# Optimization experiments

Measured on AMD Instinct MI355X. Metric: run time of the kernel, lower is better.

The kernel has to match this reference:

```python
import jax, jax.numpy as jnp
import numpy as np

EMA_W = 0.99


def setup_inputs() -> dict:
    key = jax.random.key(0)
    k1, k2 = jax.random.split(key)
    B, C, H, W = 16, 8, 512, 512
    generated_masks = jax.random.normal(k1, (B, C, H, W), dtype=jnp.float32)
    prev_dist = jax.random.uniform(k2, (C,), dtype=jnp.float32)
    prev_dist = prev_dist / jnp.sum(prev_dist)  # a valid running distribution
    return {"generated_masks": generated_masks, "prev_dist": prev_dist}


def reference(generated_masks, prev_dist):
    # generated_masks: [B, C, H, W]; prev_dist: [C]
    B, C, H, W = generated_masks.shape
    num_classes = C
    norm_factor = 1.0 / num_classes

    # per-pixel argmax over channels -> [B, H, W]
    mask_classes = jnp.argmax(generated_masks, axis=1)

    # histogram over classes (fused equivalent of torch.unique + scatter)
    hist = jnp.zeros((num_classes,), dtype=jnp.float32).at[
        mask_classes.reshape(-1)
    ].add(1.0)

    total = B * H * W
    class_distribution = prev_dist * EMA_W + (1.0 - EMA_W) * hist / total

    balance = jnp.linalg.norm(
        (class_distribution - norm_factor) / (1.0 - norm_factor)
    )
    return balance, class_distribution
```

## Files before the change

kernel.cpp:

```cpp
#include <hip/hip_runtime.h>
#include <math.h>

#define HW      262144
#define HWQ     65536
#define CHW     2097152
#define NGROUPS 1048576
#define NBLOCKS 1024
#define NTHREADS 256
#define TOTAL_PX 4194304.0f

__global__ __launch_bounds__(NTHREADS)
void argmax_hist_kernel(const float* __restrict__ masks,
                        unsigned int* __restrict__ partial) {
    const int tid = threadIdx.x;
    int cnt[8] = {0, 0, 0, 0, 0, 0, 0, 0};

    for (int g = blockIdx.x * NTHREADS + tid; g < NGROUPS; g += NBLOCKS * NTHREADS) {
        const int b   = g >> 16;
        const int hw4 = (g & 65535) << 2;
        const float4* p = (const float4*)(masks + (size_t)b * CHW + hw4);

        float4 v = p[0];
        float bv0 = v.x, bv1 = v.y, bv2 = v.z, bv3 = v.w;
        int   bi0 = 0,   bi1 = 0,   bi2 = 0,   bi3 = 0;
        #pragma unroll
        for (int c = 1; c < 8; ++c) {
            float4 u = p[(size_t)c * HWQ];
            bi0 = (u.x > bv0) ? c : bi0;  bv0 = (u.x > bv0) ? u.x : bv0;
            bi1 = (u.y > bv1) ? c : bi1;  bv1 = (u.y > bv1) ? u.y : bv1;
            bi2 = (u.z > bv2) ? c : bi2;  bv2 = (u.z > bv2) ? u.z : bv2;
            bi3 = (u.w > bv3) ? c : bi3;  bv3 = (u.w > bv3) ? u.w : bv3;
        }
        #pragma unroll
        for (int k = 0; k < 8; ++k) {
            cnt[k] += (bi0 == k) + (bi1 == k) + (bi2 == k) + (bi3 == k);
        }
    }

    #pragma unroll
    for (int k = 0; k < 8; ++k) {
        #pragma unroll
        for (int off = 32; off >= 1; off >>= 1) {
            cnt[k] += __shfl_down(cnt[k], off, 64);
        }
    }

    __shared__ int lds[32];
    const int lane = tid & 63;
    const int wid  = tid >> 6;
    if (lane == 0) {
        #pragma unroll
        for (int k = 0; k < 8; ++k) lds[wid * 8 + k] = cnt[k];
    }
    __syncthreads();
    if (tid < 8) {
        unsigned int s = (unsigned int)(lds[tid] + lds[8 + tid] + lds[16 + tid] + lds[24 + tid]);
        partial[blockIdx.x * 8 + tid] = s;
    }
}

__global__ __launch_bounds__(64)
void finalize_kernel(const unsigned int* __restrict__ partial,
                     const float* __restrict__ prev,
                     float* __restrict__ out) {
    __shared__ float s[64];
    const int t = threadIdx.x;
    const int c = t & 7;
    const int r = t >> 3;

    unsigned int sum = 0;
    for (int row = r; row < NBLOCKS; row += 8) {
        sum += partial[row * 8 + c];
    }
    s[t] = (float)sum;
    __syncthreads();

    if (t < 8) {
        float h = 0.0f;
        #pragma unroll
        for (int k = 0; k < 8; ++k) h += s[t + 8 * k];
        float dist = prev[t] * 0.99f + 0.01f * h / TOTAL_PX;
        out[1 + t] = dist;
        float d = (dist - 0.125f) / 0.875f;
        s[t] = d * d;
    }
    __syncthreads();
    if (t == 0) {
        float acc = 0.0f;
        #pragma unroll
        for (int k = 0; k < 8; ++k) acc += s[k];
        out[0] = sqrtf(acc);
    }
}

extern "C" void kernel_launch(void* const* d_in, const int* in_sizes, int n_in,
                              void* d_out, int out_size, void* d_ws, size_t ws_size,
                              hipStream_t stream) {
    const float* masks = (const float*)d_in[0];
    const float* prev  = (const float*)d_in[1];
    float* out = (float*)d_out;
    unsigned int* partial = (unsigned int*)d_ws;

    argmax_hist_kernel<<<NBLOCKS, NTHREADS, 0, stream>>>(masks, partial);
    finalize_kernel<<<1, 64, 0, stream>>>(partial, prev, out);
}
```

Baseline: 205.3 us.

## Issue all eight channel loads upfront and double grid size with fixed two-iteration loop

The argmax kernel now issues all eight float4 channel loads before any comparisons, so more memory requests are in flight per thread. The grid doubles to 2048 blocks, each thread handles exactly two fully unrolled groups, and launch bounds ask for higher occupancy. The finalize kernel widens to 256 threads to reduce the larger partial array. This raises register pressure from holding 32 floats at once, and the larger partial buffer makes the single-block finalize step longer.

```diff
diff --git a/kernel.cpp b/kernel.cpp
--- a/kernel.cpp
+++ b/kernel.cpp
@@ -1,36 +1,51 @@
 #include <hip/hip_runtime.h>
 #include <math.h>
 
-#define HW      262144
-#define HWQ     65536
-#define CHW     2097152
-#define NGROUPS 1048576
-#define NBLOCKS 1024
-#define NTHREADS 256
-#define TOTAL_PX 4194304.0f
+#define HW        262144
+#define HWQ       65536
+#define CHW       2097152
+#define NGROUPS   1048576
+#define NBLOCKS   2048
+#define NTHREADS  256
+#define GSTRIDE   524288
+#define TOTAL_PX  4194304.0f
 
-__global__ __launch_bounds__(NTHREADS)
+__global__ __launch_bounds__(NTHREADS, 8)
 void argmax_hist_kernel(const float* __restrict__ masks,
                         unsigned int* __restrict__ partial) {
     const int tid = threadIdx.x;
     int cnt[8] = {0, 0, 0, 0, 0, 0, 0, 0};
 
-    for (int g = blockIdx.x * NTHREADS + tid; g < NGROUPS; g += NBLOCKS * NTHREADS) {
+    const int gbase = blockIdx.x * NTHREADS + tid;
+
+    #pragma unroll
+    for (int it = 0; it < 2; ++it) {
+        const int g   = gbase + it * GSTRIDE;
         const int b   = g >> 16;
         const int hw4 = (g & 65535) << 2;
         const float4* p = (const float4*)(masks + (size_t)b * CHW + hw4);
 
-        float4 v = p[0];
-        float bv0 = v.x, bv1 = v.y, bv2 = v.z, bv3 = v.w;
-        int   bi0 = 0,   bi1 = 0,   bi2 = 0,   bi3 = 0;
-        #pragma unroll
-        for (int c = 1; c < 8; ++c) {
-            float4 u = p[(size_t)c * HWQ];
-            bi0 = (u.x > bv0) ? c : bi0;  bv0 = (u.x > bv0) ? u.x : bv0;
-            bi1 = (u.y > bv1) ? c : bi1;  bv1 = (u.y > bv1) ? u.y : bv1;
-            bi2 = (u.z > bv2) ? c : bi2;  bv2 = (u.z > bv2) ? u.z : bv2;
-            bi3 = (u.w > bv3) ? c : bi3;  bv3 = (u.w > bv3) ? u.w : bv3;
-        }
+        float4 v0 = p[0];
+        float4 v1 = p[1 * HWQ];
+        float4 v2 = p[2 * HWQ];
+        float4 v3 = p[3 * HWQ];
+        float4 v4 = p[4 * HWQ];
+        float4 v5 = p[5 * HWQ];
+        float4 v6 = p[6 * HWQ];
+        float4 v7 = p[7 * HWQ];
+
+        float bv0 = v0.x, bv1 = v0.y, bv2 = v0.z, bv3 = v0.w;
+        int   bi0 = 0,    bi1 = 0,    bi2 = 0,    bi3 = 0;
+
+        #define STEP(vv, c)                                                   \
+            bi0 = ((vv).x > bv0) ? (c) : bi0;  bv0 = ((vv).x > bv0) ? (vv).x : bv0; \
+            bi1 = ((vv).y > bv1) ? (c) : bi1;  bv1 = ((vv).y > bv1) ? (vv).y : bv1; \
+            bi2 = ((vv).z > bv2) ? (c) : bi2;  bv2 = ((vv).z > bv2) ? (vv).z : bv2; \
+            bi3 = ((vv).w > bv3) ? (c) : bi3;  bv3 = ((vv).w > bv3) ? (vv).w : bv3;
+        STEP(v1, 1) STEP(v2, 2) STEP(v3, 3) STEP(v4, 4)
+        STEP(v5, 5) STEP(v6, 6) STEP(v7, 7)
+        #undef STEP
+
         #pragma unroll
         for (int k = 0; k < 8; ++k) {
             cnt[k] += (bi0 == k) + (bi1 == k) + (bi2 == k) + (bi3 == k);
@@ -59,17 +74,17 @@
     }
 }
 
-__global__ __launch_bounds__(64)
+__global__ __launch_bounds__(256)
 void finalize_kernel(const unsigned int* __restrict__ partial,
                      const float* __restrict__ prev,
                      float* __restrict__ out) {
-    __shared__ float s[64];
+    __shared__ float s[256];
     const int t = threadIdx.x;
     const int c = t & 7;
-    const int r = t >> 3;
+    const int j = t >> 3;
 
     unsigned int sum = 0;
-    for (int row = r; row < NBLOCKS; row += 8) {
+    for (int row = j; row < NBLOCKS; row += 32) {
         sum += partial[row * 8 + c];
     }
     s[t] = (float)sum;
@@ -78,7 +93,7 @@
     if (t < 8) {
         float h = 0.0f;
         #pragma unroll
-        for (int k = 0; k < 8; ++k) h += s[t + 8 * k];
+        for (int k = 0; k < 32; ++k) h += s[t + 8 * k];
         float dist = prev[t] * 0.99f + 0.01f * h / TOTAL_PX;
         out[1 + t] = dist;
         float d = (dist - 0.125f) / 0.875f;
@@ -102,5 +117,5 @@
     unsigned int* partial = (unsigned int*)d_ws;
 
     argmax_hist_kernel<<<NBLOCKS, NTHREADS, 0, stream>>>(masks, partial);
-    finalize_kernel<<<1, 64, 0, stream>>>(partial, prev, out);
+    finalize_kernel<<<1, 256, 0, stream>>>(partial, prev, out);
 }
```

After: 198.9 us. 3.1% less time.
